# Optimization experiments

Measured on AMD Instinct MI355X. Metric: run time of the kernel, lower is better.

Reference implementation:

```python
import jax, jax.numpy as jnp
import numpy as np

N, C, H, K = 4096, 512, 128, 3
NEG = -jnp.inf


def _linear(x, W, b):
    return x @ W.T + b


def _lrelu(x):
    return jnp.where(x > 0, x, 0.01 * x)  # nn.LeakyReLU default slope


def _cos_sim(x, y):
    # torch cal_cos_similarity: xy / (|x| |y|^T), NaN (0/0) -> 0
    xy = x @ y.T
    den = jnp.linalg.norm(x, axis=1, keepdims=True) * jnp.linalg.norm(y, axis=1, keepdims=True).T
    return xy / jnp.where(den == 0, 1.0, den)


def setup_inputs() -> dict:
    key = jax.random.key(0)
    ks = jax.random.split(key, 24)
    x_hidden = jax.random.normal(ks[0], (N, H), jnp.float32)
    cm = (jax.random.uniform(ks[1], (N, C)) < 0.05).astype(jnp.float32)
    # ensure every concept has at least one member stock (no empty concepts)
    cm = cm.at[jnp.arange(C) % N, jnp.arange(C)].set(1.0)
    market_value = jax.random.uniform(ks[2], (N,), jnp.float32, 0.1, 1.0)
    s = 1.0 / np.sqrt(H)
    inp = {"x_hidden": x_hidden, "concept_matrix": cm, "market_value": market_value}
    names = ["ps", "ps_fore", "ps_back", "hs", "hs_fore", "hs_back", "indi"]
    for i, n in enumerate(names):
        inp[f"W_{n}"] = jax.random.uniform(ks[3 + 2 * i], (H, H), jnp.float32, -s, s)
        inp[f"b_{n}"] = jax.random.uniform(ks[4 + 2 * i], (H,), jnp.float32, -s, s)
    inp["W_out"] = jax.random.uniform(ks[20], (1, H), jnp.float32, -s, s)
    inp["b_out"] = jax.random.uniform(ks[21], (1,), jnp.float32, -s, s)
    return inp


def reference(x_hidden, concept_matrix, market_value,
              W_ps, b_ps, W_ps_fore, b_ps_fore, W_ps_back, b_ps_back,
              W_hs, b_hs, W_hs_fore, b_hs_fore, W_hs_back, b_hs_back,
              W_indi, b_indi, W_out, b_out):
    x = x_hidden
    n = x.shape[0]
    # --- predefined-concept (ps) branch ---
    s2c = concept_matrix * market_value[:, None]                     # [N,C]
    s2c_den = s2c.sum(0)[None, :] * concept_matrix + 1.0
    s2c = s2c / s2c_den
    hidden = s2c.T @ x                                               # [C,H]
    valid1 = hidden.sum(1) != 0                                      # row-filter mask
    s2c2 = jax.nn.softmax(x @ hidden.T, axis=0)                      # softmax over stocks
    hidden = (s2c2.T @ x) * valid1[:, None]                          # [C,H]
    c2s = jax.nn.softmax(jnp.where(valid1[None, :], _cos_sim(x, hidden), NEG), axis=1)
    p_shared = _linear(c2s @ hidden, W_ps, b_ps)
    p_back = _linear(p_shared, W_ps_back, b_ps_back)
    out_ps = _lrelu(_linear(p_shared, W_ps_fore, b_ps_fore))
    # --- hidden-concept (hs) branch ---
    h = x - p_back
    hs2c = _cos_sim(h, h)                                            # [N,N]
    diag = jnp.diagonal(hs2c)
    hs2c = hs2c * (1.0 - jnp.eye(n, dtype=h.dtype))
    idx = jax.lax.top_k(hs2c, K)[1]                                  # [N,K]
    mask = jnp.zeros((n, n), h.dtype).at[jnp.arange(n)[:, None], idx].set(1.0)
    hs2c = hs2c * mask
    hs2c = hs2c + jnp.diag((hs2c.sum(0) != 0).astype(h.dtype) * diag)
    hidden2 = hs2c.T @ h                                             # [N,H]
    valid2 = hidden2.sum(1) != 0
    hidden2 = hidden2 * valid2[:, None]
    hc2s = jax.nn.softmax(jnp.where(valid2[None, :], _cos_sim(h, hidden2), NEG), axis=1)
    h_shared = _linear(hc2s @ hidden2, W_hs, b_hs)
    h_back = _linear(h_shared, W_hs_back, b_hs_back)
    out_hs = _lrelu(_linear(h_shared, W_hs_fore, b_hs_fore))
    # --- individual branch ---
    indiv = x - p_back - h_back
    out_indi = _lrelu(_linear(indiv, W_indi, b_indi))
    all_info = out_ps + out_hs + out_indi
    return _linear(all_info, W_out, b_out).squeeze()                 # [N]
```

## Files before the change

kernel.cpp:

```cpp
#include <hip/hip_runtime.h>
#include <hip/hip_fp16.h>
#include <math.h>

#define N 4096
#define C 512
#define H 128
#define PAD 40
#define WP 136
#define FWP 136
#define SP 136

typedef __attribute__((ext_vector_type(8))) short bf16x8;
typedef __attribute__((ext_vector_type(4))) float f32x4;


__device__ inline float wave_reduce_sum(float v) {
#pragma unroll
  for (int m = 32; m; m >>= 1) v += __shfl_xor(v, m);
  return v;
}

__device__ inline float lrelu(float v) { return v > 0.f ? v : 0.01f * v; }

__device__ inline bool better(float v, int j, float w, int k) {
// ... 3 lines not shown
__device__ inline void top3_ins(float v, int j, float& v0, int& j0,
                                float& v1, int& j1, float& v2, int& j2) {
  if (better(v, j, v0, j0)) { v2 = v1; j2 = j1; v1 = v0; j1 = j0; v0 = v; j0 = j; }
  else if (better(v, j, v1, j1)) { v2 = v1; j2 = j1; v1 = v; j1 = j; }
  else if (better(v, j, v2, j2)) { v2 = v; j2 = j; }
}

__device__ inline void ins5(float s, int j, float v[5], int jx[5]) {
  if (!better(s, j, v[4], jx[4])) return;
  if (better(s, j, v[0], jx[0])) {
    v[4]=v[3]; jx[4]=jx[3]; v[3]=v[2]; jx[3]=jx[2]; v[2]=v[1]; jx[2]=jx[1];
    v[1]=v[0]; jx[1]=jx[0]; v[0]=s; jx[0]=j;
  } else if (better(s, j, v[1], jx[1])) {
    v[4]=v[3]; jx[4]=jx[3]; v[3]=v[2]; jx[3]=jx[2]; v[2]=v[1]; jx[2]=jx[1];
    v[1]=s; jx[1]=j;
  } else if (better(s, j, v[2], jx[2])) {
    v[4]=v[3]; jx[4]=jx[3]; v[3]=v[2]; jx[3]=jx[2]; v[2]=s; jx[2]=j;
  } else if (better(s, j, v[3], jx[3])) {
    v[4]=v[3]; jx[4]=jx[3]; v[3]=s; jx[3]=j;
  } else {
    v[4]=s; jx[4]=j;
  }
}

__device__ inline unsigned short f2bf(float f) {
  unsigned u = __float_as_uint(f);
  unsigned r = u + 0x7fffu + ((u >> 16) & 1u);
  return (unsigned short)(r >> 16);
}
__device__ inline float bf2f(unsigned short h) {
  return __uint_as_float(((unsigned)h) << 16);
}

__global__ __launch_bounds__(256) void k_split(const float* __restrict__ in,
                                               unsigned short* __restrict__ hi,
                                               unsigned short* __restrict__ lo,
                                               float* __restrict__ nrm) {
  int t = threadIdx.x;
  int idx = (blockIdx.x * 256 + t) * 4;
  float4 v = *(const float4*)&in[idx];
  float vv[4] = {v.x, v.y, v.z, v.w};
  unsigned short h[4], l[4];
  float ss = 0.f;
#pragma unroll
  for (int c = 0; c < 4; c++) {
    ss += vv[c] * vv[c];
    h[c] = f2bf(vv[c]);
    l[c] = f2bf(vv[c] - bf2f(h[c]));
  }
  uint2 ph = {(unsigned)h[0] | ((unsigned)h[1] << 16),
              (unsigned)h[2] | ((unsigned)h[3] << 16)};
  uint2 pl = {(unsigned)l[0] | ((unsigned)l[1] << 16),
              (unsigned)l[2] | ((unsigned)l[3] << 16)};
  *(uint2*)&hi[idx] = ph;
  *(uint2*)&lo[idx] = pl;
  if (nrm) {
#pragma unroll
    for (int m = 16; m; m >>= 1) ss += __shfl_xor(ss, m);
    if ((t & 31) == 0) nrm[idx >> 7] = sqrtf(ss);
  }
}

__global__ __launch_bounds__(256) void k_tsplit(const float* __restrict__ in,
                                                unsigned short* __restrict__ thi,
                                                unsigned short* __restrict__ tlo,
                                                int R) {
  __shared__ float tile[32][132];
  int r0 = blockIdx.x * 32, tid = threadIdx.x;
#pragma unroll
  for (int q = 0; q < 4; q++) {
    int f = q * 256 + tid;
    int row = f >> 5, ch = f & 31;
    *(float4*)&tile[row][ch * 4] = *(const float4*)&in[(size_t)(r0 + row) * 128 + ch * 4];
  }
  __syncthreads();
  int c = tid & 127, half = tid >> 7;
  unsigned short hh[16], ll[16];
#pragma unroll
  for (int rr = 0; rr < 16; rr++) {
    float v = tile[half * 16 + rr][c];
    hh[rr] = f2bf(v);
    ll[rr] = f2bf(v - bf2f(hh[rr]));
  }
  size_t off = (size_t)c * R + r0 + half * 16;
  uint4 ph0 = {(unsigned)hh[0] | ((unsigned)hh[1] << 16), (unsigned)hh[2] | ((unsigned)hh[3] << 16),
               (unsigned)hh[4] | ((unsigned)hh[5] << 16), (unsigned)hh[6] | ((unsigned)hh[7] << 16)};
  uint4 ph1 = {(unsigned)hh[8] | ((unsigned)hh[9] << 16), (unsigned)hh[10] | ((unsigned)hh[11] << 16),
               (unsigned)hh[12] | ((unsigned)hh[13] << 16), (unsigned)hh[14] | ((unsigned)hh[15] << 16)};
  uint4 pl0 = {(unsigned)ll[0] | ((unsigned)ll[1] << 16), (unsigned)ll[2] | ((unsigned)ll[3] << 16),
               (unsigned)ll[4] | ((unsigned)ll[5] << 16), (unsigned)ll[6] | ((unsigned)ll[7] << 16)};
  uint4 pl1 = {(unsigned)ll[8] | ((unsigned)ll[9] << 16), (unsigned)ll[10] | ((unsigned)ll[11] << 16),
               (unsigned)ll[12] | ((unsigned)ll[13] << 16), (unsigned)ll[14] | ((unsigned)ll[15] << 16)};
  *(uint4*)&thi[off] = ph0; *(uint4*)&thi[off + 8] = ph1;
// ... 33 lines not shown
  for (int s = 128; s; s >>= 1) { if (t < s) red[t] += red[t + s]; __syncthreads(); }
  if (t == 0) { colmax[c] = m; colsum[c] = red[0]; }
}

__global__ __launch_bounds__(256) void k_cs_softmax(
    const float* __restrict__ sc, const float* __restrict__ xnorm,
    const float* __restrict__ hnorm, const float* __restrict__ valid1,
    unsigned short* __restrict__ cshi, unsigned short* __restrict__ cslo) {
  __shared__ float red[256];
  int i = blockIdx.x, t = threadIdx.x;
  float xn = xnorm[i];
  float r0 = sc[(size_t)i * C + t], r1 = sc[(size_t)i * C + 256 + t];
  float d0 = xn * hnorm[t], d1 = xn * hnorm[256 + t];
  float c0 = r0 / (d0 == 0.f ? 1.f : d0);
  float c1 = r1 / (d1 == 0.f ? 1.f : d1);
  float s0 = (valid1[t] != 0.f) ? c0 : -3e38f;
  float s1 = (valid1[256 + t] != 0.f) ? c1 : -3e38f;
  red[t] = fmaxf(s0, s1); __syncthreads();
  for (int s = 128; s; s >>= 1) { if (t < s) red[t] = fmaxf(red[t], red[t + s]); __syncthreads(); }
  float m = red[0]; __syncthreads();
  float p0 = (s0 > -1e37f) ? __expf(s0 - m) : 0.f;
  float p1 = (s1 > -1e37f) ? __expf(s1 - m) : 0.f;
  red[t] = p0 + p1; __syncthreads();
  for (int s = 128; s; s >>= 1) { if (t < s) red[t] += red[t + s]; __syncthreads(); }
  float inv = 1.f / red[0];
  float a = p0 * inv, b = p1 * inv;
  unsigned short ha = f2bf(a), hb = f2bf(b);
  cshi[(size_t)i * C + t] = ha;
  cslo[(size_t)i * C + t] = f2bf(a - bf2f(ha));
  cshi[(size_t)i * C + 256 + t] = hb;
  cslo[(size_t)i * C + 256 + t] = f2bf(b - bf2f(hb));
}

__global__ __launch_bounds__(64) void k_fin_hidden2(
    const float* __restrict__ h, const float* __restrict__ diagv,
    const float* __restrict__ colsum_m, float* __restrict__ hidden2,
    unsigned short* __restrict__ h2hi, unsigned short* __restrict__ h2lo,
    float* __restrict__ valid2f) {
  int j = blockIdx.x, t = threadIdx.x;
  float add = (colsum_m[j] != 0.f) ? diagv[j] : 0.f;
  float a = hidden2[(size_t)j * H + t] + add * h[(size_t)j * H + t];
  float b = hidden2[(size_t)j * H + 64 + t] + add * h[(size_t)j * H + 64 + t];
  float s = a + b, ss = a * a + b * b;
#pragma unroll
  for (int m = 32; m; m >>= 1) { s += __shfl_xor(s, m); ss += __shfl_xor(ss, m); }
  bool valid = (s != 0.f);
  a = valid ? a : 0.f; b = valid ? b : 0.f;
  hidden2[(size_t)j * H + t] = a;
  hidden2[(size_t)j * H + 64 + t] = b;
  float inv = (valid && ss > 0.f) ? (1.f / sqrtf(ss)) : 1.f;
  float va = a * inv, vb = b * inv;
  unsigned short ha = f2bf(va), hb = f2bf(vb);
  h2hi[(size_t)j * H + t] = ha;
  h2lo[(size_t)j * H + t] = f2bf(va - bf2f(ha));
  h2hi[(size_t)j * H + 64 + t] = hb;
  h2lo[(size_t)j * H + 64 + t] = f2bf(vb - bf2f(hb));
  if (t == 0) valid2f[j] = valid ? 1.f : 0.f;
}

__global__ __launch_bounds__(256) void k_mfma_nt(
    const unsigned short* __restrict__ Ahi, const unsigned short* __restrict__ Alo,
    const unsigned short* __restrict__ Bhi, const unsigned short* __restrict__ Blo,
    float* __restrict__ out, int Nn) {
  __shared__ __align__(16) unsigned short sAh[64 * PAD];
  __shared__ __align__(16) unsigned short sAl[64 * PAD];
  __shared__ __align__(16) unsigned short sBh[128 * PAD];
  __shared__ __align__(16) unsigned short sBl[128 * PAD];
  int tid = threadIdx.x;
  int bm = blockIdx.y * 64, bn = blockIdx.x * 128;
  int lane = tid & 63, w = tid >> 6;
  int wm = (w & 1) * 32, wn = (w >> 1) * 64;
  int l15 = lane & 15, quad = lane >> 4;
  f32x4 zero = {0.f, 0.f, 0.f, 0.f};
  f32x4 acc[2][4];
#pragma unroll
  for (int mt = 0; mt < 2; mt++)
#pragma unroll
    for (int nt = 0; nt < 4; nt++) acc[mt][nt] = zero;

  for (int kt = 0; kt < 128; kt += 32) {
    {
      int row = tid >> 2, ch = tid & 3;
      size_t ga = (size_t)(bm + row) * 128 + kt + ch * 8;
      int ls = row * PAD + ch * 8;
      *(uint4*)&sAh[ls] = *(const uint4*)&Ahi[ga];
      *(uint4*)&sAl[ls] = *(const uint4*)&Alo[ga];
    }
#pragma unroll
    for (int q = 0; q < 2; q++) {
      int f = q * 256 + tid;
// ... 102 lines not shown
    for (int nt = 0; nt < 4; nt++) {
      int coll = wn + nt * 16 + l15;
#pragma unroll
      for (int rg = 0; rg < 4; rg++) {
        int rowl = wm + mt * 16 + quad * 4 + rg;
        float v = (bm + rowl == bn + coll) ? 0.f : acc[mt][nt][rg];
        sS[rowl * SP + coll] = __half_as_ushort(__float2half(v));
      }
    }
  __syncthreads();
  int r = tid >> 2, qf = tid & 3;
  const unsigned short* rowp = &sS[r * SP + qf * 32];
  int cbase = bn + qf * 32;
  float v5[5] = {-3e38f, -3e38f, -3e38f, -3e38f, -3e38f};
  int j5[5] = {0x7fffffff, 0x7fffffff, 0x7fffffff, 0x7fffffff, 0x7fffffff};
#pragma unroll
  for (int q = 0; q < 4; q++) {
    uint4 p = *(const uint4*)&rowp[q * 8];
    unsigned pk[4] = {p.x, p.y, p.z, p.w};
#pragma unroll
    for (int c2 = 0; c2 < 4; c2++) {
      float e0 = __half2float(__ushort_as_half((unsigned short)(pk[c2] & 0xffffu)));
      float e1 = __half2float(__ushort_as_half((unsigned short)(pk[c2] >> 16)));
      ins5(e0, cbase + q * 8 + c2 * 2, v5, j5);
      ins5(e1, cbase + q * 8 + c2 * 2 + 1, v5, j5);
    }
  }
  int slot = (bn >> 5) + qf;
  float2* cp = &cand[((size_t)(bm + r) * 128 + slot) * 5];
#pragma unroll
  for (int c2 = 0; c2 < 5; c2++) cp[c2] = {v5[c2], __int_as_float(j5[c2])};
}

__global__ __launch_bounds__(256) void k_rowtop2(
    const float2* __restrict__ cand, const float* __restrict__ hhat,
    float* __restrict__ mtv, int* __restrict__ mtj) {
  int i = blockIdx.x * 4 + (threadIdx.x >> 6);
  int lane = threadIdx.x & 63;
  const float2* cr = &cand[(size_t)i * 640];
  float v[5] = {-3e38f, -3e38f, -3e38f, -3e38f, -3e38f};
  int jx[5] = {0x7fffffff, 0x7fffffff, 0x7fffffff, 0x7fffffff, 0x7fffffff};
#pragma unroll
  for (int c = 0; c < 10; c++) {
    float2 p = cr[lane * 10 + c];
    ins5(p.x, __float_as_int(p.y), v, jx);
  }
#pragma unroll
  for (int d = 1; d < 64; d <<= 1) {
    float fv[5]; int fj[5];
#pragma unroll
    for (int c = 0; c < 5; c++) { fv[c] = __shfl_xor(v[c], d); fj[c] = __shfl_xor(jx[c], d); }
#pragma unroll
    for (int c = 0; c < 5; c++) ins5(fv[c], fj[c], v, jx);
  }
  const float* hi = &hhat[(size_t)i * H];
  float b0 = -3e38f, b1 = -3e38f, b2 = -3e38f;
  int q0 = 0, q1 = 0, q2 = 0;
#pragma unroll
  for (int c = 0; c < 5; c++) {
    int j = jx[c];
    float s;
    if (j == i) {
      s = 0.f;
    } else {
      const float* hj = &hhat[(size_t)j * H];
      float p = hi[lane] * hj[lane] + hi[lane + 64] * hj[lane + 64];
      s = wave_reduce_sum(p);
    }
    top3_ins(s, j, b0, q0, b1, q1, b2, q2);
  }
  if (lane == 0) {
    mtv[i * 3 + 0] = b0; mtv[i * 3 + 1] = b1; mtv[i * 3 + 2] = b2;
    mtj[i * 3 + 0] = q0; mtj[i * 3 + 1] = q1; mtj[i * 3 + 2] = q2;
  }
}

__global__ __launch_bounds__(512) void k_flash(
    const unsigned short* __restrict__ Qhi, const unsigned short* __restrict__ Qlo,
    const unsigned short* __restrict__ Khi, const unsigned short* __restrict__ Klo,
    const unsigned short* __restrict__ Vthi, const unsigned short* __restrict__ Vtlo,
    const float* __restrict__ valid2f, float* __restrict__ partialU,
    float* __restrict__ plsum, int KVC) {
  __shared__ __align__(16) unsigned short sQh[128 * FWP];
  __shared__ __align__(16) unsigned short sQl[128 * FWP];
  __shared__ __align__(16) unsigned short sP[128 * FWP];
  __shared__ __align__(16) unsigned short sBh[2][128 * PAD];
  __shared__ __align__(16) unsigned short sBl[2][128 * PAD];
  __shared__ float lsum_s[128];
  int tid = threadIdx.x;
  int z = blockIdx.x;
  int bm = blockIdx.y * 128;
  int j0 = z * KVC;
  int lane = tid & 63, w = tid >> 6;
  int wm = (w & 3) * 32, wn = (w >> 2) * 64;
  int l15 = lane & 15, quad = lane >> 4;
  int srow = tid >> 2, sch = tid & 3;
  int sls = srow * PAD + sch * 8;
#pragma unroll
  for (int q = 0; q < 4; q++) {
    int f = q * 512 + tid;
    int row = f >> 4, ch = f & 15;
    size_t ga = (size_t)(bm + row) * 128 + ch * 8;
    int ls = row * FWP + ch * 8;
    *(uint4*)&sQh[ls] = *(const uint4*)&Qhi[ga];
    *(uint4*)&sQl[ls] = *(const uint4*)&Qlo[ga];
  }
// ... 277 lines not shown
#pragma unroll
    for (int t = 0; t < 4; t++) {
      int ar = (wm + t * 16 + l15) * PAD + quad * 8;
      ah[t] = *(const bf16x8*)&sAh[ar];
      al[t] = *(const bf16x8*)&sAl[ar];
      int br = (wn + t * 16 + l15) * PAD + quad * 8;
      bh[t] = *(const bf16x8*)&sBh[br];
      bl[t] = *(const bf16x8*)&sBl[br];
    }
#pragma unroll
    for (int mt = 0; mt < 4; mt++)
#pragma unroll
      for (int nt = 0; nt < 4; nt++) {
        acc[mt][nt] = __builtin_amdgcn_mfma_f32_16x16x32_bf16(ah[mt], bh[nt], acc[mt][nt], 0, 0, 0);
        acc[mt][nt] = __builtin_amdgcn_mfma_f32_16x16x32_bf16(ah[mt], bl[nt], acc[mt][nt], 0, 0, 0);
        acc[mt][nt] = __builtin_amdgcn_mfma_f32_16x16x32_bf16(al[mt], bh[nt], acc[mt][nt], 0, 0, 0);
      }
    __syncthreads();
  }
  float* pp = partial + (size_t)blockIdx.z * C * 128;
#pragma unroll
  for (int mt = 0; mt < 4; mt++)
#pragma unroll
    for (int nt = 0; nt < 4; nt++) {
      int col = wn + nt * 16 + l15;
#pragma unroll
      for (int rg = 0; rg < 4; rg++) {
        int row = bm + wm + mt * 16 + quad * 4 + rg;
        pp[(size_t)row * 128 + col] = acc[mt][nt][rg];
      }
    }
}

__global__ __launch_bounds__(256) void k_scatter(
    const float* __restrict__ mtv, const int* __restrict__ mtj,
    const float* __restrict__ h, float* __restrict__ hidden2,
    float* __restrict__ colsum_m) {
  int i = blockIdx.x * 4 + (threadIdx.x >> 6);
  int lane = threadIdx.x & 63;
  float h0 = h[(size_t)i * H + lane], h1 = h[(size_t)i * H + 64 + lane];
#pragma unroll
  for (int s = 0; s < 3; s++) {
    float v = mtv[i * 3 + s];
    int j = mtj[i * 3 + s];
    atomicAdd(&hidden2[(size_t)j * H + lane], v * h0);
    atomicAdd(&hidden2[(size_t)j * H + 64 + lane], v * h1);
    if (lane == s) atomicAdd(&colsum_m[j], v);
  }
}

__global__ __launch_bounds__(256) void k_reduce(
    const float* __restrict__ partial, float* __restrict__ out, int cnt,
    size_t slot, size_t size4, const float* __restrict__ scalem,
    const float* __restrict__ plsum, unsigned short* __restrict__ hi,
    unsigned short* __restrict__ lo, float* __restrict__ nrmout,
    float* __restrict__ validout) {
  size_t idx = (size_t)blockIdx.x * 256 + threadIdx.x;
  if (idx >= size4) return;
  float4 s = {0, 0, 0, 0};
  for (int c = 0; c < cnt; c++) {
    float4 v = *(const float4*)&partial[c * slot + idx * 4];
    s.x += v.x; s.y += v.y; s.z += v.z; s.w += v.w;
  }
  if (scalem) {
    float sc = scalem[idx >> 5];
    s.x *= sc; s.y *= sc; s.z *= sc; s.w *= sc;
  }
  if (plsum) {
    int r = idx >> 5;
    float d = 0.f;
    for (int c = 0; c < cnt; c++) d += plsum[(size_t)c * N + r];
    float sc = 1.f / d;
    s.x *= sc; s.y *= sc; s.z *= sc; s.w *= sc;
  }
  *(float4*)&out[idx * 4] = s;
  if (hi) {
    float vv[4] = {s.x, s.y, s.z, s.w};
    unsigned short h[4], l[4];
#pragma unroll
    for (int c = 0; c < 4; c++) {
      h[c] = f2bf(vv[c]);
      l[c] = f2bf(vv[c] - bf2f(h[c]));
    }
    uint2 ph = {(unsigned)h[0] | ((unsigned)h[1] << 16),
                (unsigned)h[2] | ((unsigned)h[3] << 16)};
    uint2 pl = {(unsigned)l[0] | ((unsigned)l[1] << 16),
                (unsigned)l[2] | ((unsigned)l[3] << 16)};
    *(uint2*)&hi[idx * 4] = ph;
    *(uint2*)&lo[idx * 4] = pl;
  }
  if (nrmout || validout) {
    float rs = s.x + s.y + s.z + s.w;
    float rq = s.x * s.x + s.y * s.y + s.z * s.z + s.w * s.w;
#pragma unroll
    for (int m = 16; m; m >>= 1) { rs += __shfl_xor(rs, m); rq += __shfl_xor(rq, m); }
    if ((threadIdx.x & 31) == 0) {
      if (nrmout) nrmout[idx >> 5] = sqrtf(rq);
      if (validout) validout[idx >> 5] = (rs != 0.f) ? 1.f : 0.f;
    }
  }
}


#define LOAD_W(Wt)                                                        \
  do {                                                                    \
    _Pragma("unroll") for (int q = 0; q < 16; q++) {                      \
      int f = q * 256 + tid;                                              \
      int wr = f >> 5, wc = (f & 31) * 4;                                 \
      float4 wv = *(const float4*)&(Wt)[(size_t)wr * 128 + wc];           \
      float ww[4] = {wv.x, wv.y, wv.z, wv.w};                             \
      _Pragma("unroll") for (int c = 0; c < 4; c++) {                     \
        unsigned short hh = f2bf(ww[c]);                                  \
        sWh[wr * WP + wc + c] = hh;                                       \
        sWl[wr * WP + wc + c] = f2bf(ww[c] - bf2f(hh));                   \
      }                                                                   \
    }                                                                     \
  } while (0)

#define GEMM32(accv)                                                              \
  do {                                                                            \
    _Pragma("unroll") for (int nt = 0; nt < 4; nt++) accv[nt] = zero;             \
    _Pragma("unroll") for (int kt = 0; kt < 128; kt += 32) {                      \
      bf16x8 ah = *(const bf16x8*)&sAh[(rt + l15) * WP + kt + quad * 8];          \
      bf16x8 al = *(const bf16x8*)&sAl[(rt + l15) * WP + kt + quad * 8];          \
      _Pragma("unroll") for (int nt = 0; nt < 4; nt++) {                          \
        int br = (ch2 + nt * 16 + l15) * WP + kt + quad * 8;                      \
        bf16x8 bh = *(const bf16x8*)&sWh[br];                                     \
        bf16x8 bl = *(const bf16x8*)&sWl[br];                                     \
        accv[nt] = __builtin_amdgcn_mfma_f32_16x16x32_bf16(ah, bh, accv[nt], 0, 0, 0); \
        accv[nt] = __builtin_amdgcn_mfma_f32_16x16x32_bf16(ah, bl, accv[nt], 0, 0, 0); \
        accv[nt] = __builtin_amdgcn_mfma_f32_16x16x32_bf16(al, bh, accv[nt], 0, 0, 0); \
      }                                                                           \
    }                                                                             \
  } while (0)

__global__ __launch_bounds__(256) void k_ps_tail(
    const float* __restrict__ A, const float* __restrict__ x,
    const float* __restrict__ W_ps, const float* __restrict__ b_ps,
    const float* __restrict__ W_psb, const float* __restrict__ b_psb,
    const float* __restrict__ W_psf, const float* __restrict__ b_psf,
    float* __restrict__ hbuf, float* __restrict__ hhat,
    unsigned short* __restrict__ hhi, unsigned short* __restrict__ hlo,
    float* __restrict__ diagv, float* __restrict__ all_info) {
  __shared__ __align__(16) unsigned short sWh[128 * WP];
  __shared__ __align__(16) unsigned short sWl[128 * WP];
  __shared__ __align__(16) unsigned short sAh[32 * WP];
  __shared__ __align__(16) unsigned short sAl[32 * WP];
  __shared__ __align__(16) float sF[32][132];
  int tid = threadIdx.x;
  int bm = blockIdx.x * 32;
  int lane = tid & 63, w = tid >> 6;
  int rt = (w & 1) * 16, ch2 = (w >> 1) * 64;
  int l15 = lane & 15, quad = lane >> 4;
  f32x4 zero = {0.f, 0.f, 0.f, 0.f};
  f32x4 acc[4];

  {
    int row = tid >> 3, c0 = (tid & 7) * 16;
    const float* src = &A[(size_t)(bm + row) * 128 + c0];
#pragma unroll
    for (int q = 0; q < 4; q++) {
      float4 v = *(const float4*)&src[q * 4];
      float vv[4] = {v.x, v.y, v.z, v.w};
#pragma unroll
      for (int c = 0; c < 4; c++) {
        unsigned short hh = f2bf(vv[c]);
        sAh[row * WP + c0 + q * 4 + c] = hh;
        sAl[row * WP + c0 + q * 4 + c] = f2bf(vv[c] - bf2f(hh));
      }
    }
  }
  LOAD_W(W_ps);
  __syncthreads();
  GEMM32(acc);
  __syncthreads();
#pragma unroll
  for (int nt = 0; nt < 4; nt++) {
    int col = ch2 + nt * 16 + l15;
    float bv = b_ps[col];
#pragma unroll
    for (int rg = 0; rg < 4; rg++) {
      int row = rt + quad * 4 + rg;
      float v = acc[nt][rg] + bv;
      unsigned short hh = f2bf(v);
      sAh[row * WP + col] = hh;
      sAl[row * WP + col] = f2bf(v - bf2f(hh));
    }
  }
  LOAD_W(W_psb);
  __syncthreads();
  GEMM32(acc);
#pragma unroll
  for (int nt = 0; nt < 4; nt++) {
    int col = ch2 + nt * 16 + l15;
    float bv = b_psb[col];
#pragma unroll
// ... 37 lines not shown
    for (int q4 = 0; q4 < 4; q4++) {
      float4 fv = {va16[q4 * 4], va16[q4 * 4 + 1], va16[q4 * 4 + 2], va16[q4 * 4 + 3]};
      *(float4*)&hhat[base + q4 * 4] = fv;
    }
    uint4 ph0 = {(unsigned)hh16[0] | ((unsigned)hh16[1] << 16), (unsigned)hh16[2] | ((unsigned)hh16[3] << 16),
                 (unsigned)hh16[4] | ((unsigned)hh16[5] << 16), (unsigned)hh16[6] | ((unsigned)hh16[7] << 16)};
    uint4 ph1 = {(unsigned)hh16[8] | ((unsigned)hh16[9] << 16), (unsigned)hh16[10] | ((unsigned)hh16[11] << 16),
                 (unsigned)hh16[12] | ((unsigned)hh16[13] << 16), (unsigned)hh16[14] | ((unsigned)hh16[15] << 16)};
    uint4 pl0 = {(unsigned)ll16[0] | ((unsigned)ll16[1] << 16), (unsigned)ll16[2] | ((unsigned)ll16[3] << 16),
                 (unsigned)ll16[4] | ((unsigned)ll16[5] << 16), (unsigned)ll16[6] | ((unsigned)ll16[7] << 16)};
    uint4 pl1 = {(unsigned)ll16[8] | ((unsigned)ll16[9] << 16), (unsigned)ll16[10] | ((unsigned)ll16[11] << 16),
                 (unsigned)ll16[12] | ((unsigned)ll16[13] << 16), (unsigned)ll16[14] | ((unsigned)ll16[15] << 16)};
    *(uint4*)&hhi[base] = ph0; *(uint4*)&hhi[base + 8] = ph1;
    *(uint4*)&hlo[base] = pl0; *(uint4*)&hlo[base + 8] = pl1;
    if ((tid & 7) == 0) diagv[bm + row] = dg;
  }
  LOAD_W(W_psf);
  __syncthreads();
  GEMM32(acc);
#pragma unroll
  for (int nt = 0; nt < 4; nt++) {
    int col = ch2 + nt * 16 + l15;
    float bv = b_psf[col];
#pragma unroll
    for (int rg = 0; rg < 4; rg++) {
      int row = rt + quad * 4 + rg;
      size_t off = (size_t)(bm + row) * 128 + col;
      all_info[off] = lrelu(acc[nt][rg] + bv);
    }
  }
}

__global__ __launch_bounds__(256) void k_hs_tail(
    const float* __restrict__ A, const float* __restrict__ hbuf,
    const float* __restrict__ all_info,
    const float* __restrict__ W_hs, const float* __restrict__ b_hs,
    const float* __restrict__ W_hsf, const float* __restrict__ b_hsf,
    const float* __restrict__ W_hsb, const float* __restrict__ b_hsb,
    const float* __restrict__ W_in, const float* __restrict__ b_in,
    const float* __restrict__ W_out, const float* __restrict__ b_out,
    float* __restrict__ out) {
  __shared__ __align__(16) unsigned short sWh[128 * WP];
  __shared__ __align__(16) unsigned short sWl[128 * WP];
  __shared__ __align__(16) unsigned short sAh[32 * WP];
  __shared__ __align__(16) unsigned short sAl[32 * WP];
  __shared__ __align__(16) float sF[32][132];
  int tid = threadIdx.x;
  int bm = blockIdx.x * 32;
  int lane = tid & 63, w = tid >> 6;
  int rt = (w & 1) * 16, ch2 = (w >> 1) * 64;
  int l15 = lane & 15, quad = lane >> 4;
  f32x4 zero = {0.f, 0.f, 0.f, 0.f};
  f32x4 acc[4];
  float allv[4][4];

  {
    int row = tid >> 3, c0 = (tid & 7) * 16;
    const float* src = &A[(size_t)(bm + row) * 128 + c0];
#pragma unroll
    for (int q = 0; q < 4; q++) {
      float4 v = *(const float4*)&src[q * 4];
      float vv[4] = {v.x, v.y, v.z, v.w};
#pragma unroll
      for (int c = 0; c < 4; c++) {
        unsigned short hh = f2bf(vv[c]);
        sAh[row * WP + c0 + q * 4 + c] = hh;
        sAl[row * WP + c0 + q * 4 + c] = f2bf(vv[c] - bf2f(hh));
      }
    }
  }
  LOAD_W(W_hs);
  __syncthreads();
  GEMM32(acc);
  __syncthreads();
#pragma unroll
  for (int nt = 0; nt < 4; nt++) {
    int col = ch2 + nt * 16 + l15;
    float bv = b_hs[col];
#pragma unroll
    for (int rg = 0; rg < 4; rg++) {
      int row = rt + quad * 4 + rg;
      float v = acc[nt][rg] + bv;
      unsigned short hh = f2bf(v);
      sAh[row * WP + col] = hh;
      sAl[row * WP + col] = f2bf(v - bf2f(hh));
    }
  }
  LOAD_W(W_hsf);
  __syncthreads();
  GEMM32(acc);
#pragma unroll
  for (int nt = 0; nt < 4; nt++) {
    int col = ch2 + nt * 16 + l15;
    float bv = b_hsf[col];
#pragma unroll
    for (int rg = 0; rg < 4; rg++) {
      int row = rt + quad * 4 + rg;
      size_t off = (size_t)(bm + row) * 128 + col;
      allv[nt][rg] = all_info[off] + lrelu(acc[nt][rg] + bv);
    }
// ... 54 lines not shown
}


extern "C" void kernel_launch(void* const* d_in, const int* in_sizes, int n_in,
                              void* d_out, int out_size, void* d_ws, size_t ws_size,
                              hipStream_t stream) {
  (void)in_sizes; (void)n_in; (void)out_size; (void)ws_size;
  const float* x   = (const float*)d_in[0];
  const float* cm  = (const float*)d_in[1];
  const float* mv  = (const float*)d_in[2];
  const float* W_ps = (const float*)d_in[3],  *b_ps = (const float*)d_in[4];
  const float* W_psf = (const float*)d_in[5], *b_psf = (const float*)d_in[6];
  const float* W_psb = (const float*)d_in[7], *b_psb = (const float*)d_in[8];
  const float* W_hs = (const float*)d_in[9],  *b_hs = (const float*)d_in[10];
  const float* W_hsf = (const float*)d_in[11], *b_hsf = (const float*)d_in[12];
  const float* W_hsb = (const float*)d_in[13], *b_hsb = (const float*)d_in[14];
  const float* W_in = (const float*)d_in[15], *b_in = (const float*)d_in[16];
  const float* W_out = (const float*)d_in[17], *b_out = (const float*)d_in[18];
  float* out = (float*)d_out;

  float* W = (float*)d_ws;
  size_t o = 0;
  auto alloc = [&](size_t n) { float* p = W + o; o += n; return p; };
  float* colsum_c = alloc(C);
  float* colmax   = alloc(C);
  float* colsumexp= alloc(C);
  float* valid1   = alloc(C);
  float* hnorm_ps = alloc(C);
  float* xnorm    = alloc(N);
  float* diagv    = alloc(N);
  float* colsum_m = alloc(N);
  float* valid2f  = alloc(N);
  float* plsum    = alloc((size_t)8 * N);
  float* mtv      = alloc(3 * N);
  int*   mtj      = (int*)alloc(3 * N);
  float* hidden1  = alloc((size_t)C * H);
  float* hidden_ps= alloc((size_t)C * H);
  float* scores   = alloc((size_t)N * C);
  float* ps_pre   = alloc((size_t)N * H);
  float* all_info = alloc((size_t)N * H);
  float* hbuf     = alloc((size_t)N * H);
  float* hhat     = alloc((size_t)N * H);
  float* hidden2  = alloc((size_t)N * H);
  unsigned short* xhi    = (unsigned short*)alloc((size_t)N * H / 2);
  unsigned short* xlo    = (unsigned short*)alloc((size_t)N * H / 2);
  unsigned short* hhathi = (unsigned short*)alloc((size_t)N * H / 2);
  unsigned short* hhatlo = (unsigned short*)alloc((size_t)N * H / 2);
  unsigned short* h2hi   = (unsigned short*)alloc((size_t)N * H / 2);
  unsigned short* h2lo   = (unsigned short*)alloc((size_t)N * H / 2);
  unsigned short* h1hi   = (unsigned short*)alloc((size_t)C * H / 2);
  unsigned short* h1lo   = (unsigned short*)alloc((size_t)C * H / 2);
  unsigned short* hpshi  = (unsigned short*)alloc((size_t)C * H / 2);
  unsigned short* hpslo  = (unsigned short*)alloc((size_t)C * H / 2);
  unsigned short* cshi   = (unsigned short*)alloc((size_t)N * C / 2);
  unsigned short* cslo   = (unsigned short*)alloc((size_t)N * C / 2);
  unsigned short* hpst_hi= (unsigned short*)alloc((size_t)H * C / 2);
  unsigned short* hpst_lo= (unsigned short*)alloc((size_t)H * C / 2);
  unsigned short* h2t_hi = (unsigned short*)alloc((size_t)H * N / 2);
  unsigned short* h2t_lo = (unsigned short*)alloc((size_t)H * N / 2);
  unsigned short* xt_hi  = (unsigned short*)alloc((size_t)H * N / 2);
  unsigned short* xt_lo  = (unsigned short*)alloc((size_t)H * N / 2);
  float2* cand    = (float2*)alloc((size_t)N * 128 * 5 * 2);
  float* partial  = W + o;
  const int Z = 8;
  const int ZG = 64;
  const int ZK = 8;

  hipMemsetAsync(colsum_c, 0, C * sizeof(float), stream);
  hipMemsetAsync(colsum_m, 0, N * sizeof(float), stream);
  hipMemsetAsync(hidden2, 0, (size_t)N * H * sizeof(float), stream);

  dim3 blk(256);
  k_split<<<dim3(N * H / 1024), blk, 0, stream>>>(x, xhi, xlo, xnorm);
  k_tsplit<<<dim3(N / 32), blk, 0, stream>>>(x, xt_hi, xt_lo, N);
  k_colsum_s2c<<<dim3(C / 64, 16), dim3(64), 0, stream>>>(cm, mv, colsum_c);
  k_mfma_genA<1><<<dim3(1, C / 128, ZG), blk, 0, stream>>>(
      cm, mv, colsum_c, nullptr, xt_hi, xt_lo, partial, N / ZG);
  k_reduce<<<dim3(C * H / 4 / 256), blk, 0, stream>>>(
      partial, hidden1, ZG, (size_t)C * H, (size_t)C * H / 4, nullptr, nullptr,
      h1hi, h1lo, nullptr, valid1);
  k_mfma_nt<<<dim3(C / 128, N / 64), blk, 0, stream>>>(
      xhi, xlo, h1hi, h1lo, scores, C);
  k_colstats<<<dim3(C), blk, 0, stream>>>(scores, colmax, colsumexp);
  k_mfma_genA<2><<<dim3(1, C / 128, ZG), blk, 0, stream>>>(
      scores, nullptr, colmax, colsumexp, xt_hi, xt_lo, partial, N / ZG);
  k_reduce<<<dim3(C * H / 4 / 256), blk, 0, stream>>>(
      partial, hidden_ps, ZG, (size_t)C * H, (size_t)C * H / 4, valid1, nullptr,
      hpshi, hpslo, hnorm_ps, nullptr);
  k_mfma_nt<<<dim3(C / 128, N / 64), blk, 0, stream>>>(
      xhi, xlo, hpshi, hpslo, scores, C);
  k_cs_softmax<<<dim3(N), blk, 0, stream>>>(scores, xnorm, hnorm_ps, valid1,
                                            cshi, cslo);
  k_tsplit<<<dim3(C / 32), blk, 0, stream>>>(hidden_ps, hpst_hi, hpst_lo, C);
  k_mfma_kn<<<dim3(1, N / 128, ZK), blk, 0, stream>>>(
      cshi, cslo, hpst_hi, hpst_lo, partial, C, C / ZK);
  k_reduce<<<dim3(N * H / 4 / 256), blk, 0, stream>>>(
      partial, ps_pre, ZK, (size_t)N * H, (size_t)N * H / 4, nullptr, nullptr,
      nullptr, nullptr, nullptr, nullptr);
  k_ps_tail<<<dim3(N / 32), blk, 0, stream>>>(
      ps_pre, x, W_ps, b_ps, W_psb, b_psb, W_psf, b_psf,
      hbuf, hhat, hhathi, hhatlo, diagv, all_info);
  k_snt<<<dim3(N / 128, N / 128), dim3(512), 0, stream>>>(
      hhathi, hhatlo, cand);
  k_rowtop2<<<dim3(N / 4), blk, 0, stream>>>(cand, hhat, mtv, mtj);
  k_scatter<<<dim3(N / 4), blk, 0, stream>>>(mtv, mtj, hbuf, hidden2, colsum_m);
  k_fin_hidden2<<<dim3(N), dim3(64), 0, stream>>>(hbuf, diagv, colsum_m, hidden2,
                                                  h2hi, h2lo, valid2f);
  k_tsplit<<<dim3(N / 32), blk, 0, stream>>>(hidden2, h2t_hi, h2t_lo, N);
  k_flash<<<dim3(Z, N / 128), dim3(512), 0, stream>>>(
      hhathi, hhatlo, h2hi, h2lo, h2t_hi, h2t_lo, valid2f, partial, plsum,
      N / Z);
  k_reduce<<<dim3(N * H / 4 / 256), blk, 0, stream>>>(
      partial, ps_pre, Z, (size_t)N * H, (size_t)N * H / 4, nullptr, plsum,
      nullptr, nullptr, nullptr, nullptr);
  k_hs_tail<<<dim3(N / 32), blk, 0, stream>>>(
      ps_pre, hbuf, all_info, W_hs, b_hs, W_hsf, b_hsf, W_hsb, b_hsb,
      W_in, b_in, W_out, b_out, out);
}
```

Before: 369.2 us.

## Fuse prep, scatter, finalize/transpose, and split-K reductions into neighbouring kernels

Merges the x split and transpose-split into one kernel that also zeroes hidden2 and the column-sum buffers, which replaces three memsets. The top-3 selection kernel now does the atomic scatter itself, so the mtv/mtj buffers go away. The hidden2 finalize and its transpose-split become one 32-row tiled kernel. The split-K partial reductions, including the flash-attention row normaliser, move into the ps and hs tail kernels. Together this drops about seven launches and several N×H round trips through global memory, at the cost of longer per-thread loops in the tails.

```diff
diff --git a/kernel.cpp b/kernel.cpp
--- a/kernel.cpp
+++ b/kernel.cpp
@@ -59,33 +59,71 @@
   return __uint_as_float(((unsigned)h) << 16);
 }
 
-__global__ __launch_bounds__(256) void k_split(const float* __restrict__ in,
-                                               unsigned short* __restrict__ hi,
-                                               unsigned short* __restrict__ lo,
-                                               float* __restrict__ nrm) {
-  int t = threadIdx.x;
-  int idx = (blockIdx.x * 256 + t) * 4;
-  float4 v = *(const float4*)&in[idx];
-  float vv[4] = {v.x, v.y, v.z, v.w};
-  unsigned short h[4], l[4];
-  float ss = 0.f;
-#pragma unroll
-  for (int c = 0; c < 4; c++) {
-    ss += vv[c] * vv[c];
-    h[c] = f2bf(vv[c]);
-    l[c] = f2bf(vv[c] - bf2f(h[c]));
-  }
-  uint2 ph = {(unsigned)h[0] | ((unsigned)h[1] << 16),
-              (unsigned)h[2] | ((unsigned)h[3] << 16)};
-  uint2 pl = {(unsigned)l[0] | ((unsigned)l[1] << 16),
-              (unsigned)l[2] | ((unsigned)l[3] << 16)};
-  *(uint2*)&hi[idx] = ph;
-  *(uint2*)&lo[idx] = pl;
-  if (nrm) {
+__global__ __launch_bounds__(256) void k_xprep(
+    const float* __restrict__ in, unsigned short* __restrict__ hi,
+    unsigned short* __restrict__ lo, float* __restrict__ nrm,
+    unsigned short* __restrict__ thi, unsigned short* __restrict__ tlo,
+    float* __restrict__ hidden2, float* __restrict__ colsum_c,
+    float* __restrict__ colsum_m) {
+  __shared__ float tile[32][132];
+  int r0 = blockIdx.x * 32, tid = threadIdx.x;
+  float4 zf = {0.f, 0.f, 0.f, 0.f};
+#pragma unroll
+  for (int q = 0; q < 4; q++) {
+    size_t zi = ((size_t)blockIdx.x * 1024 + q * 256 + tid) * 4;
+    *(float4*)&hidden2[zi] = zf;
+  }
+  if (blockIdx.x == 0 && tid < 128) *(float4*)&colsum_c[tid * 4] = zf;
+  if (blockIdx.x == 1) {
+#pragma unroll
+    for (int q = 0; q < 4; q++) *(float4*)&colsum_m[(q * 256 + tid) * 4] = zf;
+  }
+#pragma unroll
+  for (int q = 0; q < 4; q++) {
+    int f = q * 256 + tid;
+    int row = f >> 5, ch = f & 31;
+    size_t gi = (size_t)(r0 + row) * 128 + ch * 4;
+    float4 v = *(const float4*)&in[gi];
+    *(float4*)&tile[row][ch * 4] = v;
+    float vv[4] = {v.x, v.y, v.z, v.w};
+    unsigned short hq[4], lq[4];
+    float ss = 0.f;
+#pragma unroll
+    for (int c = 0; c < 4; c++) {
+      ss += vv[c] * vv[c];
+      hq[c] = f2bf(vv[c]);
+      lq[c] = f2bf(vv[c] - bf2f(hq[c]));
+    }
+    uint2 ph = {(unsigned)hq[0] | ((unsigned)hq[1] << 16),
+                (unsigned)hq[2] | ((unsigned)hq[3] << 16)};
+    uint2 pl = {(unsigned)lq[0] | ((unsigned)lq[1] << 16),
+                (unsigned)lq[2] | ((unsigned)lq[3] << 16)};
+    *(uint2*)&hi[gi] = ph;
+    *(uint2*)&lo[gi] = pl;
 #pragma unroll
     for (int m = 16; m; m >>= 1) ss += __shfl_xor(ss, m);
-    if ((t & 31) == 0) nrm[idx >> 7] = sqrtf(ss);
-  }
+    if ((tid & 31) == 0) nrm[r0 + row] = sqrtf(ss);
+  }
+  __syncthreads();
+  int c = tid & 127, half = tid >> 7;
+  unsigned short hh[16], ll[16];
+#pragma unroll
+  for (int rr = 0; rr < 16; rr++) {
+    float v = tile[half * 16 + rr][c];
+    hh[rr] = f2bf(v);
+    ll[rr] = f2bf(v - bf2f(hh[rr]));
+  }
+  size_t off = (size_t)c * N + r0 + half * 16;
+  uint4 ph0 = {(unsigned)hh[0] | ((unsigned)hh[1] << 16), (unsigned)hh[2] | ((unsigned)hh[3] << 16),
+               (unsigned)hh[4] | ((unsigned)hh[5] << 16), (unsigned)hh[6] | ((unsigned)hh[7] << 16)};
+  uint4 ph1 = {(unsigned)hh[8] | ((unsigned)hh[9] << 16), (unsigned)hh[10] | ((unsigned)hh[11] << 16),
+               (unsigned)hh[12] | ((unsigned)hh[13] << 16), (unsigned)hh[14] | ((unsigned)hh[15] << 16)};
+  uint4 pl0 = {(unsigned)ll[0] | ((unsigned)ll[1] << 16), (unsigned)ll[2] | ((unsigned)ll[3] << 16),
+               (unsigned)ll[4] | ((unsigned)ll[5] << 16), (unsigned)ll[6] | ((unsigned)ll[7] << 16)};
+  uint4 pl1 = {(unsigned)ll[8] | ((unsigned)ll[9] << 16), (unsigned)ll[10] | ((unsigned)ll[11] << 16),
+               (unsigned)ll[12] | ((unsigned)ll[13] << 16), (unsigned)ll[14] | ((unsigned)ll[15] << 16)};
+  *(uint4*)&thi[off] = ph0; *(uint4*)&thi[off + 8] = ph1;
+  *(uint4*)&tlo[off] = pl0; *(uint4*)&tlo[off + 8] = pl1;
 }
 
 __global__ __launch_bounds__(256) void k_tsplit(const float* __restrict__ in,
@@ -185,30 +223,75 @@
   cslo[(size_t)i * C + 256 + t] = f2bf(b - bf2f(hb));
 }
 
-__global__ __launch_bounds__(64) void k_fin_hidden2(
+__global__ __launch_bounds__(256) void k_fin2t(
     const float* __restrict__ h, const float* __restrict__ diagv,
     const float* __restrict__ colsum_m, float* __restrict__ hidden2,
     unsigned short* __restrict__ h2hi, unsigned short* __restrict__ h2lo,
-    float* __restrict__ valid2f) {
-  int j = blockIdx.x, t = threadIdx.x;
+    float* __restrict__ valid2f, unsigned short* __restrict__ thi,
+    unsigned short* __restrict__ tlo) {
+  __shared__ float tile[32][132];
+  int j0 = blockIdx.x * 32, tid = threadIdx.x;
+  int row = tid >> 3, c0 = (tid & 7) * 16;
+  int j = j0 + row;
   float add = (colsum_m[j] != 0.f) ? diagv[j] : 0.f;
-  float a = hidden2[(size_t)j * H + t] + add * h[(size_t)j * H + t];
-  float b = hidden2[(size_t)j * H + 64 + t] + add * h[(size_t)j * H + 64 + t];
-  float s = a + b, ss = a * a + b * b;
-#pragma unroll
-  for (int m = 32; m; m >>= 1) { s += __shfl_xor(s, m); ss += __shfl_xor(ss, m); }
+  float a16[16];
+  float s = 0.f, ss = 0.f;
+#pragma unroll
+  for (int q = 0; q < 16; q++) {
+    float a = hidden2[(size_t)j * H + c0 + q] + add * h[(size_t)j * H + c0 + q];
+    a16[q] = a;
+    s += a; ss += a * a;
+  }
+#pragma unroll
+  for (int m = 4; m; m >>= 1) { s += __shfl_xor(s, m); ss += __shfl_xor(ss, m); }
   bool valid = (s != 0.f);
-  a = valid ? a : 0.f; b = valid ? b : 0.f;
-  hidden2[(size_t)j * H + t] = a;
-  hidden2[(size_t)j * H + 64 + t] = b;
   float inv = (valid && ss > 0.f) ? (1.f / sqrtf(ss)) : 1.f;
-  float va = a * inv, vb = b * inv;
-  unsigned short ha = f2bf(va), hb = f2bf(vb);
-  h2hi[(size_t)j * H + t] = ha;
-  h2lo[(size_t)j * H + t] = f2bf(va - bf2f(ha));
-  h2hi[(size_t)j * H + 64 + t] = hb;
-  h2lo[(size_t)j * H + 64 + t] = f2bf(vb - bf2f(hb));
-  if (t == 0) valid2f[j] = valid ? 1.f : 0.f;
+  size_t base = (size_t)j * H + c0;
+  unsigned short hh16[16], ll16[16];
+#pragma unroll
+  for (int q = 0; q < 16; q++) {
+    a16[q] = valid ? a16[q] : 0.f;
+    float va = a16[q] * inv;
+    hh16[q] = f2bf(va);
+    ll16[q] = f2bf(va - bf2f(hh16[q]));
+    tile[row][c0 + q] = a16[q];
+  }
+#pragma unroll
+  for (int q4 = 0; q4 < 4; q4++) {
+    float4 fv = {a16[q4 * 4], a16[q4 * 4 + 1], a16[q4 * 4 + 2], a16[q4 * 4 + 3]};
+    *(float4*)&hidden2[base + q4 * 4] = fv;
+  }
+  uint4 ph0 = {(unsigned)hh16[0] | ((unsigned)hh16[1] << 16), (unsigned)hh16[2] | ((unsigned)hh16[3] << 16),
+               (unsigned)hh16[4] | ((unsigned)hh16[5] << 16), (unsigned)hh16[6] | ((unsigned)hh16[7] << 16)};
+  uint4 ph1 = {(unsigned)hh16[8] | ((unsigned)hh16[9] << 16), (unsigned)hh16[10] | ((unsigned)hh16[11] << 16),
+               (unsigned)hh16[12] | ((unsigned)hh16[13] << 16), (unsigned)hh16[14] | ((unsigned)hh16[15] << 16)};
+  uint4 pl0 = {(unsigned)ll16[0] | ((unsigned)ll16[1] << 16), (unsigned)ll16[2] | ((unsigned)ll16[3] << 16),
+               (unsigned)ll16[4] | ((unsigned)ll16[5] << 16), (unsigned)ll16[6] | ((unsigned)ll16[7] << 16)};
+  uint4 pl1 = {(unsigned)ll16[8] | ((unsigned)ll16[9] << 16), (unsigned)ll16[10] | ((unsigned)ll16[11] << 16),
+               (unsigned)ll16[12] | ((unsigned)ll16[13] << 16), (unsigned)ll16[14] | ((unsigned)ll16[15] << 16)};
+  *(uint4*)&h2hi[base] = ph0; *(uint4*)&h2hi[base + 8] = ph1;
+  *(uint4*)&h2lo[base] = pl0; *(uint4*)&h2lo[base + 8] = pl1;
+  if ((tid & 7) == 0) valid2f[j] = valid ? 1.f : 0.f;
+  __syncthreads();
+  int c = tid & 127, half = tid >> 7;
+  unsigned short th[16], tl[16];
+#pragma unroll
+  for (int rr = 0; rr < 16; rr++) {
+    float v = tile[half * 16 + rr][c];
+    th[rr] = f2bf(v);
+    tl[rr] = f2bf(v - bf2f(th[rr]));
+  }
+  size_t off = (size_t)c * N + j0 + half * 16;
+  uint4 tp0 = {(unsigned)th[0] | ((unsigned)th[1] << 16), (unsigned)th[2] | ((unsigned)th[3] << 16),
+               (unsigned)th[4] | ((unsigned)th[5] << 16), (unsigned)th[6] | ((unsigned)th[7] << 16)};
+  uint4 tp1 = {(unsigned)th[8] | ((unsigned)th[9] << 16), (unsigned)th[10] | ((unsigned)th[11] << 16),
+               (unsigned)th[12] | ((unsigned)th[13] << 16), (unsigned)th[14] | ((unsigned)th[15] << 16)};
+  uint4 tq0 = {(unsigned)tl[0] | ((unsigned)tl[1] << 16), (unsigned)tl[2] | ((unsigned)tl[3] << 16),
+               (unsigned)tl[4] | ((unsigned)tl[5] << 16), (unsigned)tl[6] | ((unsigned)tl[7] << 16)};
+  uint4 tq1 = {(unsigned)tl[8] | ((unsigned)tl[9] << 16), (unsigned)tl[10] | ((unsigned)tl[11] << 16),
+               (unsigned)tl[12] | ((unsigned)tl[13] << 16), (unsigned)tl[14] | ((unsigned)tl[15] << 16)};
+  *(uint4*)&thi[off] = tp0; *(uint4*)&thi[off + 8] = tp1;
+  *(uint4*)&tlo[off] = tq0; *(uint4*)&tlo[off + 8] = tq1;
 }
 
 __global__ __launch_bounds__(256) void k_mfma_nt(
@@ -377,9 +460,10 @@
   for (int c2 = 0; c2 < 5; c2++) cp[c2] = {v5[c2], __int_as_float(j5[c2])};
 }
 
-__global__ __launch_bounds__(256) void k_rowtop2(
+__global__ __launch_bounds__(256) void k_rowtop2s(
     const float2* __restrict__ cand, const float* __restrict__ hhat,
-    float* __restrict__ mtv, int* __restrict__ mtj) {
+    const float* __restrict__ h, float* __restrict__ hidden2,
+    float* __restrict__ colsum_m) {
   int i = blockIdx.x * 4 + (threadIdx.x >> 6);
   int lane = threadIdx.x & 63;
   const float2* cr = &cand[(size_t)i * 640];
@@ -414,9 +498,16 @@
     }
     top3_ins(s, j, b0, q0, b1, q1, b2, q2);
   }
-  if (lane == 0) {
-    mtv[i * 3 + 0] = b0; mtv[i * 3 + 1] = b1; mtv[i * 3 + 2] = b2;
-    mtj[i * 3 + 0] = q0; mtj[i * 3 + 1] = q1; mtj[i * 3 + 2] = q2;
+  float h0 = h[(size_t)i * H + lane], h1 = h[(size_t)i * H + 64 + lane];
+  float bv[3] = {b0, b1, b2};
+  int qv[3] = {q0, q1, q2};
+#pragma unroll
+  for (int s = 0; s < 3; s++) {
+    float vv = bv[s];
+    int j = qv[s];
+    atomicAdd(&hidden2[(size_t)j * H + lane], vv * h0);
+    atomicAdd(&hidden2[(size_t)j * H + 64 + lane], vv * h1);
+    if (lane == s) atomicAdd(&colsum_m[j], vv);
   }
 }
 
@@ -760,29 +851,11 @@
     }
 }
 
-__global__ __launch_bounds__(256) void k_scatter(
-    const float* __restrict__ mtv, const int* __restrict__ mtj,
-    const float* __restrict__ h, float* __restrict__ hidden2,
-    float* __restrict__ colsum_m) {
-  int i = blockIdx.x * 4 + (threadIdx.x >> 6);
-  int lane = threadIdx.x & 63;
-  float h0 = h[(size_t)i * H + lane], h1 = h[(size_t)i * H + 64 + lane];
-#pragma unroll
-  for (int s = 0; s < 3; s++) {
-    float v = mtv[i * 3 + s];
-    int j = mtj[i * 3 + s];
-    atomicAdd(&hidden2[(size_t)j * H + lane], v * h0);
-    atomicAdd(&hidden2[(size_t)j * H + 64 + lane], v * h1);
-    if (lane == s) atomicAdd(&colsum_m[j], v);
-  }
-}
-
 __global__ __launch_bounds__(256) void k_reduce(
     const float* __restrict__ partial, float* __restrict__ out, int cnt,
     size_t slot, size_t size4, const float* __restrict__ scalem,
-    const float* __restrict__ plsum, unsigned short* __restrict__ hi,
-    unsigned short* __restrict__ lo, float* __restrict__ nrmout,
-    float* __restrict__ validout) {
+    unsigned short* __restrict__ hi, unsigned short* __restrict__ lo,
+    float* __restrict__ nrmout, float* __restrict__ validout) {
   size_t idx = (size_t)blockIdx.x * 256 + threadIdx.x;
   if (idx >= size4) return;
   float4 s = {0, 0, 0, 0};
@@ -792,13 +865,6 @@
   }
   if (scalem) {
     float sc = scalem[idx >> 5];
-    s.x *= sc; s.y *= sc; s.z *= sc; s.w *= sc;
-  }
-  if (plsum) {
-    int r = idx >> 5;
-    float d = 0.f;
-    for (int c = 0; c < cnt; c++) d += plsum[(size_t)c * N + r];
-    float sc = 1.f / d;
     s.x *= sc; s.y *= sc; s.z *= sc; s.w *= sc;
   }
   *(float4*)&out[idx * 4] = s;
@@ -863,7 +929,7 @@
   } while (0)
 
 __global__ __launch_bounds__(256) void k_ps_tail(
-    const float* __restrict__ A, const float* __restrict__ x,
+    const float* __restrict__ partial, int zcnt, const float* __restrict__ x,
     const float* __restrict__ W_ps, const float* __restrict__ b_ps,
     const float* __restrict__ W_psb, const float* __restrict__ b_psb,
     const float* __restrict__ W_psf, const float* __restrict__ b_psf,
@@ -885,11 +951,14 @@
 
   {
     int row = tid >> 3, c0 = (tid & 7) * 16;
-    const float* src = &A[(size_t)(bm + row) * 128 + c0];
+    size_t off0 = (size_t)(bm + row) * 128 + c0;
 #pragma unroll
     for (int q = 0; q < 4; q++) {
-      float4 v = *(const float4*)&src[q * 4];
-      float vv[4] = {v.x, v.y, v.z, v.w};
+      float vv[4] = {0.f, 0.f, 0.f, 0.f};
+      for (int z = 0; z < zcnt; z++) {
+        float4 v = *(const float4*)&partial[(size_t)z * N * H + off0 + q * 4];
+        vv[0] += v.x; vv[1] += v.y; vv[2] += v.z; vv[3] += v.w;
+      }
 #pragma unroll
       for (int c = 0; c < 4; c++) {
         unsigned short hh = f2bf(vv[c]);
@@ -993,8 +1062,8 @@
 }
 
 __global__ __launch_bounds__(256) void k_hs_tail(
-    const float* __restrict__ A, const float* __restrict__ hbuf,
-    const float* __restrict__ all_info,
+    const float* __restrict__ partial, const float* __restrict__ plsum, int zcnt,
+    const float* __restrict__ hbuf, const float* __restrict__ all_info,
     const float* __restrict__ W_hs, const float* __restrict__ b_hs,
     const float* __restrict__ W_hsf, const float* __restrict__ b_hsf,
     const float* __restrict__ W_hsb, const float* __restrict__ b_hsb,
@@ -1017,16 +1086,23 @@
 
   {
     int row = tid >> 3, c0 = (tid & 7) * 16;
-    const float* src = &A[(size_t)(bm + row) * 128 + c0];
+    float d = 0.f;
+    for (int z = 0; z < zcnt; z++) d += plsum[(size_t)z * N + bm + row];
+    float sc = 1.f / d;
+    size_t off0 = (size_t)(bm + row) * 128 + c0;
 #pragma unroll
     for (int q = 0; q < 4; q++) {
-      float4 v = *(const float4*)&src[q * 4];
-      float vv[4] = {v.x, v.y, v.z, v.w};
+      float vv[4] = {0.f, 0.f, 0.f, 0.f};
+      for (int z = 0; z < zcnt; z++) {
+        float4 v = *(const float4*)&partial[(size_t)z * N * H + off0 + q * 4];
+        vv[0] += v.x; vv[1] += v.y; vv[2] += v.z; vv[3] += v.w;
+      }
 #pragma unroll
       for (int c = 0; c < 4; c++) {
-        unsigned short hh = f2bf(vv[c]);
+        float val = vv[c] * sc;
+        unsigned short hh = f2bf(val);
         sAh[row * WP + c0 + q * 4 + c] = hh;
-        sAl[row * WP + c0 + q * 4 + c] = f2bf(vv[c] - bf2f(hh));
+        sAl[row * WP + c0 + q * 4 + c] = f2bf(val - bf2f(hh));
       }
     }
   }
@@ -1147,12 +1223,9 @@
   float* colsum_m = alloc(N);
   float* valid2f  = alloc(N);
   float* plsum    = alloc((size_t)8 * N);
-  float* mtv      = alloc(3 * N);
-  int*   mtj      = (int*)alloc(3 * N);
   float* hidden1  = alloc((size_t)C * H);
   float* hidden_ps= alloc((size_t)C * H);
   float* scores   = alloc((size_t)N * C);
-  float* ps_pre   = alloc((size_t)N * H);
   float* all_info = alloc((size_t)N * H);
   float* hbuf     = alloc((size_t)N * H);
   float* hhat     = alloc((size_t)N * H);
@@ -1181,18 +1254,14 @@
   const int ZG = 64;
   const int ZK = 8;
 
-  hipMemsetAsync(colsum_c, 0, C * sizeof(float), stream);
-  hipMemsetAsync(colsum_m, 0, N * sizeof(float), stream);
-  hipMemsetAsync(hidden2, 0, (size_t)N * H * sizeof(float), stream);
-
   dim3 blk(256);
-  k_split<<<dim3(N * H / 1024), blk, 0, stream>>>(x, xhi, xlo, xnorm);
-  k_tsplit<<<dim3(N / 32), blk, 0, stream>>>(x, xt_hi, xt_lo, N);
+  k_xprep<<<dim3(N / 32), blk, 0, stream>>>(x, xhi, xlo, xnorm, xt_hi, xt_lo,
+                                            hidden2, colsum_c, colsum_m);
   k_colsum_s2c<<<dim3(C / 64, 16), dim3(64), 0, stream>>>(cm, mv, colsum_c);
   k_mfma_genA<1><<<dim3(1, C / 128, ZG), blk, 0, stream>>>(
       cm, mv, colsum_c, nullptr, xt_hi, xt_lo, partial, N / ZG);
   k_reduce<<<dim3(C * H / 4 / 256), blk, 0, stream>>>(
-      partial, hidden1, ZG, (size_t)C * H, (size_t)C * H / 4, nullptr, nullptr,
+      partial, hidden1, ZG, (size_t)C * H, (size_t)C * H / 4, nullptr,
       h1hi, h1lo, nullptr, valid1);
   k_mfma_nt<<<dim3(C / 128, N / 64), blk, 0, stream>>>(
       xhi, xlo, h1hi, h1lo, scores, C);
@@ -1200,7 +1269,7 @@
   k_mfma_genA<2><<<dim3(1, C / 128, ZG), blk, 0, stream>>>(
       scores, nullptr, colmax, colsumexp, xt_hi, xt_lo, partial, N / ZG);
   k_reduce<<<dim3(C * H / 4 / 256), blk, 0, stream>>>(
-      partial, hidden_ps, ZG, (size_t)C * H, (size_t)C * H / 4, valid1, nullptr,
+      partial, hidden_ps, ZG, (size_t)C * H, (size_t)C * H / 4, valid1,
       hpshi, hpslo, hnorm_ps, nullptr);
   k_mfma_nt<<<dim3(C / 128, N / 64), blk, 0, stream>>>(
       xhi, xlo, hpshi, hpslo, scores, C);
@@ -1209,26 +1278,19 @@
   k_tsplit<<<dim3(C / 32), blk, 0, stream>>>(hidden_ps, hpst_hi, hpst_lo, C);
   k_mfma_kn<<<dim3(1, N / 128, ZK), blk, 0, stream>>>(
       cshi, cslo, hpst_hi, hpst_lo, partial, C, C / ZK);
-  k_reduce<<<dim3(N * H / 4 / 256), blk, 0, stream>>>(
-      partial, ps_pre, ZK, (size_t)N * H, (size_t)N * H / 4, nullptr, nullptr,
-      nullptr, nullptr, nullptr, nullptr);
   k_ps_tail<<<dim3(N / 32), blk, 0, stream>>>(
-      ps_pre, x, W_ps, b_ps, W_psb, b_psb, W_psf, b_psf,
+      partial, ZK, x, W_ps, b_ps, W_psb, b_psb, W_psf, b_psf,
       hbuf, hhat, hhathi, hhatlo, diagv, all_info);
   k_snt<<<dim3(N / 128, N / 128), dim3(512), 0, stream>>>(
       hhathi, hhatlo, cand);
-  k_rowtop2<<<dim3(N / 4), blk, 0, stream>>>(cand, hhat, mtv, mtj);
-  k_scatter<<<dim3(N / 4), blk, 0, stream>>>(mtv, mtj, hbuf, hidden2, colsum_m);
-  k_fin_hidden2<<<dim3(N), dim3(64), 0, stream>>>(hbuf, diagv, colsum_m, hidden2,
-                                                  h2hi, h2lo, valid2f);
-  k_tsplit<<<dim3(N / 32), blk, 0, stream>>>(hidden2, h2t_hi, h2t_lo, N);
+  k_rowtop2s<<<dim3(N / 4), blk, 0, stream>>>(cand, hhat, hbuf, hidden2,
+                                              colsum_m);
+  k_fin2t<<<dim3(N / 32), blk, 0, stream>>>(hbuf, diagv, colsum_m, hidden2,
+                                            h2hi, h2lo, valid2f, h2t_hi, h2t_lo);
   k_flash<<<dim3(Z, N / 128), dim3(512), 0, stream>>>(
       hhathi, hhatlo, h2hi, h2lo, h2t_hi, h2t_lo, valid2f, partial, plsum,
       N / Z);
-  k_reduce<<<dim3(N * H / 4 / 256), blk, 0, stream>>>(
-      partial, ps_pre, Z, (size_t)N * H, (size_t)N * H / 4, nullptr, plsum,
-      nullptr, nullptr, nullptr, nullptr);
   k_hs_tail<<<dim3(N / 32), blk, 0, stream>>>(
-      ps_pre, hbuf, all_info, W_hs, b_hs, W_hsf, b_hsf, W_hsb, b_hsb,
+      partial, plsum, Z, hbuf, all_info, W_hs, b_hs, W_hsf, b_hsf, W_hsb, b_hsb,
       W_in, b_in, W_out, b_out, out);
 }
```

New measurement: 397.7 us, median of 2. 7.7% more time.
